# Optimization experiments

Measured on AMD Instinct MI355X. Metric: run time of the kernel, lower is better.

## Reference

```python
import jax, jax.numpy as jnp
import numpy as np

# dims
P, NB, K, NNODES, NPTS, D = 128, 16, 64, 512, 20000, 256
FINEMATCH_MAX_POINT = 450


def setup_inputs() -> dict:
    key = jax.random.key(0)
    k1, k2, k3, k4, k5, k6 = jax.random.split(key, 6)
    ref_node_neighbor_mask = jax.random.uniform(k1, (P, NB)) < 0.9
    ref_node_neighbor_mask = ref_node_neighbor_mask.at[:, 0].set(True)  # ensure no empty proposals
    ref_seed_neighbor_indices = jax.random.randint(k2, (P, NB), 0, NNODES)
    ref_node_knn_masks = jax.random.uniform(k3, (NNODES, K)) < 0.7
    ref_node_knn_masks = ref_node_knn_masks.at[:, 0].set(True)
    ref_node_knn_indices = jax.random.randint(k4, (NNODES, K), 0, NPTS)
    ref_node_knn_points = jax.random.normal(k5, (NNODES, K, 3), dtype=jnp.float32)
    ref_feats_m = jax.random.normal(k6, (NPTS, D), dtype=jnp.float32)
    return {
        'ref_node_neighbor_mask': ref_node_neighbor_mask,
        'ref_seed_neighbor_indices': ref_seed_neighbor_indices,
        'ref_node_knn_masks': ref_node_knn_masks,
        'ref_node_knn_points': ref_node_knn_points,
        'ref_node_knn_indices': ref_node_knn_indices,
        'ref_feats_m': ref_feats_m,
    }


def reference(ref_node_neighbor_mask, ref_seed_neighbor_indices, ref_node_knn_masks,
              ref_node_knn_points, ref_node_knn_indices, ref_feats_m):
    num_proposal, num_neighbors = ref_seed_neighbor_indices.shape
    k = ref_node_knn_masks.shape[-1]
    L = num_neighbors * k
    d = ref_feats_m.shape[-1]
    M = FINEMATCH_MAX_POINT

    # gather per-proposal flattened groups  [P, L]
    corr_masks = ref_node_knn_masks[ref_seed_neighbor_indices].reshape(num_proposal, L)
    corr_points = ref_node_knn_points[ref_seed_neighbor_indices].reshape(num_proposal, L, 3)
    corr_indices = ref_node_knn_indices[ref_seed_neighbor_indices].reshape(num_proposal, L)

    # sentinel feature row (index == NPTS maps to zeros)
    padded_feats = jnp.concatenate([ref_feats_m, jnp.zeros((1, d), ref_feats_m.dtype)], axis=0)
    corr_feats = padded_feats[corr_indices]  # [P, L, D]

    # neighbor mask expand(P, NB, K).reshape(P, NB*K) == repeat each neighbor K times
    nb_mask = jnp.repeat(ref_node_neighbor_mask, k, axis=1)
    corr_masks = jnp.logical_and(corr_masks, nb_mask)

    # per-proposal valid counts and ordered valid positions (stable sort keeps order)
    n = corr_masks.sum(axis=1)  # [P]
    order = jnp.argsort(jnp.logical_not(corr_masks), axis=1)  # valid positions first, in order

    i = jnp.arange(M)
    # resample: floor((i/M) * n) replicates torch float32 linspace resampling
    frac = i.astype(jnp.float32) / jnp.float32(M)
    resampled = jnp.floor(frac[None, :] * n[:, None].astype(jnp.float32)).astype(jnp.int32)
    direct = jnp.broadcast_to(i[None, :].astype(jnp.int32), (num_proposal, M))
    local = jnp.where((n > M)[:, None], resampled, direct)
    out_mask = i[None, :] < jnp.minimum(n, M)[:, None]  # [P, M]
    local = jnp.clip(local, 0, L - 1)

    pos = jnp.take_along_axis(order, local, axis=1)  # [P, M] positions into flattened group
    pts = jnp.take_along_axis(corr_points, pos[:, :, None], axis=1)  # [P, M, 3]
    fts = jnp.take_along_axis(corr_feats, pos[:, :, None], axis=1)   # [P, M, D]
    zero = jnp.zeros((), pts.dtype)
    local_ref_corr_points = jnp.where(out_mask[:, :, None], pts, zero)
    local_ref_corr_feats = jnp.where(out_mask[:, :, None], fts, zero)
    return local_ref_corr_points, local_ref_corr_feats, out_mask
```

## Files before the change

### kernel.cpp

```cpp
#include <hip/hip_runtime.h>

#define NP 128
#define NB 16
#define KK 64
#define LL 1024
#define MM 450
#define DD 256

__device__ __forceinline__ bool probe_is_u8(const void* nb_mask_raw) {
    const unsigned int* w = (const unsigned int*)nb_mask_raw;
    bool u8 = false;
#pragma unroll
    for (int q = 0; q < 16; ++q) u8 |= (w[q] > 1u);
    return u8;
}

__device__ __forceinline__ int read_bool(const void* buf, int idx, bool is_u8) {
    if (is_u8) return ((const unsigned char*)buf)[idx] != 0;
    return ((const int*)buf)[idx] != 0;
}

__global__ __launch_bounds__(256) void n2p_compact(
    const void* __restrict__ nb_mask_raw,
    const int*  __restrict__ seed_idx,
    const void* __restrict__ knn_mask_raw,
    int* __restrict__ ws_order,
    int* __restrict__ ws_n)
{
    const int p = blockIdx.x;
    const int t = threadIdx.x;
    const bool is_u8 = probe_is_u8(nb_mask_raw);

    __shared__ int s_node[NB];
    __shared__ int s_m[NB];
    __shared__ int s_scan[256];

    if (t < NB) {
        s_node[t] = seed_idx[p * NB + t];
        s_m[t]    = read_bool(nb_mask_raw, p * NB + t, is_u8);
    }
    __syncthreads();

    const int base = t * 4;
    int v[4];
    int cnt = 0;
#pragma unroll
    for (int q = 0; q < 4; ++q) {
        const int l  = base + q;
        const int nb = l >> 6;
        const int k  = l & 63;
        const int valid = s_m[nb] && read_bool(knn_mask_raw, s_node[nb] * KK + k, is_u8);
        v[q] = valid;
        cnt += valid;
    }

    s_scan[t] = cnt;
    __syncthreads();
    int val = cnt;
    for (int off = 1; off < 256; off <<= 1) {
        int other = (t >= off) ? s_scan[t - off] : 0;
        __syncthreads();
        val += other;
        s_scan[t] = val;
        __syncthreads();
    }

    if (t == 255) ws_n[p] = val;

    int r = val - cnt;
#pragma unroll
    for (int q = 0; q < 4; ++q) {
        if (v[q]) ws_order[p * LL + (r++)] = base + q;
    }
}

__global__ __launch_bounds__(256) void n2p_gather(
    const int*   __restrict__ seed_idx,
    const float* __restrict__ knn_pts,
    const int*   __restrict__ knn_idx,
    const float* __restrict__ feats,
    const int*   __restrict__ ws_order,
    const int*   __restrict__ ws_n,
    float* __restrict__ out_pts,
    float* __restrict__ out_feats,
    float* __restrict__ out_mask)
{
    const int p    = blockIdx.x;
    const int wave = threadIdx.x >> 6;
    const int lane = threadIdx.x & 63;
    const int i    = blockIdx.y * 4 + wave;
    if (i >= MM) return;

    const int n     = ws_n[p];
    const int n_eff = (n < MM) ? n : MM;
    const size_t row = (size_t)p * MM + i;

    if (i < n_eff) {
        int j;
        if (n > MM) {
            j = (i * n) / MM;
        } else {
            j = i;
        }
        const int l    = ws_order[p * LL + j];
        const int nb   = l >> 6;
        const int k    = l & 63;
        const int node = seed_idx[p * NB + nb];
        const int gk   = node * KK + k;
        const int idx  = knn_idx[gk];

        const float4 f = reinterpret_cast<const float4*>(feats + (size_t)idx * DD)[lane];
        reinterpret_cast<float4*>(out_feats + row * DD)[lane] = f;

        if (lane < 3)  out_pts[row * 3 + lane] = knn_pts[(size_t)gk * 3 + lane];
        if (lane == 0) out_mask[row] = 1.0f;
    } else {
        const float4 z = make_float4(0.f, 0.f, 0.f, 0.f);
        reinterpret_cast<float4*>(out_feats + row * DD)[lane] = z;
        if (lane < 3)  out_pts[row * 3 + lane] = 0.0f;
        if (lane == 0) out_mask[row] = 0.0f;
    }
}

extern "C" void kernel_launch(void* const* d_in, const int* in_sizes, int n_in,
                              void* d_out, int out_size, void* d_ws, size_t ws_size,
                              hipStream_t stream) {
    const void*  nb_mask  = d_in[0];
    const int*   seed_idx = (const int*)d_in[1];
    const void*  knn_mask = d_in[2];
    const float* knn_pts  = (const float*)d_in[3];
    const int*   knn_idx  = (const int*)d_in[4];
    const float* feats    = (const float*)d_in[5];

    float* out_pts   = (float*)d_out;
    float* out_feats = out_pts + (size_t)NP * MM * 3;
    float* out_mask  = out_feats + (size_t)NP * MM * DD;

    int* ws_n     = (int*)d_ws;
    int* ws_order = ws_n + NP;

    n2p_compact<<<dim3(NP), dim3(256), 0, stream>>>(
        nb_mask, seed_idx, knn_mask, ws_order, ws_n);

    n2p_gather<<<dim3(NP, (MM + 3) / 4), dim3(256), 0, stream>>>(
        seed_idx, knn_pts, knn_idx, feats, ws_order, ws_n,
        out_pts, out_feats, out_mask);
}
```

Baseline: 110.7 us.

## Fuse compaction and gather into one kernel with ballot-based scan

```diff
diff --git a/kernel.cpp b/kernel.cpp
--- a/kernel.cpp
+++ b/kernel.cpp
@@ -6,6 +6,8 @@
 #define LL 1024
 #define MM 450
 #define DD 256
+#define CHUNKS 8
+#define ROWS 57
 
 __device__ __forceinline__ bool probe_is_u8(const void* nb_mask_raw) {
     const unsigned int* w = (const unsigned int*)nb_mask_raw;
@@ -20,105 +22,104 @@
     return ((const int*)buf)[idx] != 0;
 }
 
-__global__ __launch_bounds__(256) void n2p_compact(
-    const void* __restrict__ nb_mask_raw,
-    const int*  __restrict__ seed_idx,
-    const void* __restrict__ knn_mask_raw,
-    int* __restrict__ ws_order,
-    int* __restrict__ ws_n)
-{
-    const int p = blockIdx.x;
-    const int t = threadIdx.x;
-    const bool is_u8 = probe_is_u8(nb_mask_raw);
-
-    __shared__ int s_node[NB];
-    __shared__ int s_m[NB];
-    __shared__ int s_scan[256];
-
-    if (t < NB) {
-        s_node[t] = seed_idx[p * NB + t];
-        s_m[t]    = read_bool(nb_mask_raw, p * NB + t, is_u8);
-    }
-    __syncthreads();
-
-    const int base = t * 4;
-    int v[4];
-    int cnt = 0;
-#pragma unroll
-    for (int q = 0; q < 4; ++q) {
-        const int l  = base + q;
-        const int nb = l >> 6;
-        const int k  = l & 63;
-        const int valid = s_m[nb] && read_bool(knn_mask_raw, s_node[nb] * KK + k, is_u8);
-        v[q] = valid;
-        cnt += valid;
-    }
-
-    s_scan[t] = cnt;
-    __syncthreads();
-    int val = cnt;
-    for (int off = 1; off < 256; off <<= 1) {
-        int other = (t >= off) ? s_scan[t - off] : 0;
-        __syncthreads();
-        val += other;
-        s_scan[t] = val;
-        __syncthreads();
-    }
-
-    if (t == 255) ws_n[p] = val;
-
-    int r = val - cnt;
-#pragma unroll
-    for (int q = 0; q < 4; ++q) {
-        if (v[q]) ws_order[p * LL + (r++)] = base + q;
-    }
-}
-
-__global__ __launch_bounds__(256) void n2p_gather(
+__global__ __launch_bounds__(256) void n2p_fused(
+    const void*  __restrict__ nb_mask_raw,
     const int*   __restrict__ seed_idx,
+    const void*  __restrict__ knn_mask_raw,
     const float* __restrict__ knn_pts,
     const int*   __restrict__ knn_idx,
     const float* __restrict__ feats,
-    const int*   __restrict__ ws_order,
-    const int*   __restrict__ ws_n,
     float* __restrict__ out_pts,
     float* __restrict__ out_feats,
     float* __restrict__ out_mask)
 {
-    const int p    = blockIdx.x;
-    const int wave = threadIdx.x >> 6;
-    const int lane = threadIdx.x & 63;
-    const int i    = blockIdx.y * 4 + wave;
-    if (i >= MM) return;
+    const int p     = blockIdx.x;
+    const int chunk = blockIdx.y;
+    const int t     = threadIdx.x;
+    const int wv    = t >> 6;
+    const int ln    = t & 63;
 
-    const int n     = ws_n[p];
-    const int n_eff = (n < MM) ? n : MM;
-    const size_t row = (size_t)p * MM + i;
+    __shared__ int s_node[NB];
+    __shared__ int s_order[LL];
+    __shared__ int s_wsum[4];
+    __shared__ int s_src[ROWS];
+    __shared__ int s_fidx[ROWS];
 
-    if (i < n_eff) {
-        int j;
-        if (n > MM) {
-            j = (i * n) / MM;
+    const bool is_u8 = probe_is_u8(nb_mask_raw);
+
+    if (t < NB) s_node[t] = seed_idx[p * NB + t];
+    __syncthreads();
+
+    int v[4];
+#pragma unroll
+    for (int q = 0; q < 4; ++q) {
+        const int nbi  = wv * 4 + q;
+        const int node = s_node[nbi];
+        const int m_nb = read_bool(nb_mask_raw, p * NB + nbi, is_u8);
+        const int m_kn = read_bool(knn_mask_raw, node * KK + ln, is_u8);
+        v[q] = m_nb && m_kn;
+    }
+    const unsigned long long lt = (1ULL << ln) - 1ULL;
+    int my_rank[4];
+    int wtot = 0;
+#pragma unroll
+    for (int q = 0; q < 4; ++q) {
+        const unsigned long long b = __ballot(v[q] != 0);
+        my_rank[q] = wtot + __popcll(b & lt);
+        wtot += __popcll(b);
+    }
+    if (ln == 0) s_wsum[wv] = wtot;
+    __syncthreads();
+
+    int wave_off = 0;
+    for (int w2 = 0; w2 < wv; ++w2) wave_off += s_wsum[w2];
+    const int n_total = s_wsum[0] + s_wsum[1] + s_wsum[2] + s_wsum[3];
+#pragma unroll
+    for (int q = 0; q < 4; ++q) {
+        if (v[q]) s_order[wave_off + my_rank[q]] = wv * 256 + q * 64 + ln;
+    }
+    __syncthreads();
+
+    const int row0  = chunk * ROWS;
+    const int nrows = (MM - row0 < ROWS) ? (MM - row0) : ROWS;
+    const int n_eff = (n_total < MM) ? n_total : MM;
+
+    if (t < nrows) {
+        const int i = row0 + t;
+        int src = -1, fidx = -1;
+        if (i < n_eff) {
+            const int j = (n_total > MM) ? (int)((unsigned)(i * n_total) / (unsigned)MM)
+                                         : i;
+            const int l    = s_order[j];
+            const int node = s_node[l >> 6];
+            src  = node * KK + (l & 63);
+            fidx = knn_idx[src];
+        }
+        s_src[t]  = src;
+        s_fidx[t] = fidx;
+
+        const size_t row = (size_t)p * MM + i;
+        if (src >= 0) {
+            out_pts[row * 3 + 0] = knn_pts[(size_t)src * 3 + 0];
+            out_pts[row * 3 + 1] = knn_pts[(size_t)src * 3 + 1];
+            out_pts[row * 3 + 2] = knn_pts[(size_t)src * 3 + 2];
+            out_mask[row] = 1.0f;
         } else {
-            j = i;
+            out_pts[row * 3 + 0] = 0.0f;
+            out_pts[row * 3 + 1] = 0.0f;
+            out_pts[row * 3 + 2] = 0.0f;
+            out_mask[row] = 0.0f;
         }
-        const int l    = ws_order[p * LL + j];
-        const int nb   = l >> 6;
-        const int k    = l & 63;
-        const int node = seed_idx[p * NB + nb];
-        const int gk   = node * KK + k;
-        const int idx  = knn_idx[gk];
+    }
+    __syncthreads();
 
-        const float4 f = reinterpret_cast<const float4*>(feats + (size_t)idx * DD)[lane];
-        reinterpret_cast<float4*>(out_feats + row * DD)[lane] = f;
-
-        if (lane < 3)  out_pts[row * 3 + lane] = knn_pts[(size_t)gk * 3 + lane];
-        if (lane == 0) out_mask[row] = 1.0f;
-    } else {
-        const float4 z = make_float4(0.f, 0.f, 0.f, 0.f);
-        reinterpret_cast<float4*>(out_feats + row * DD)[lane] = z;
-        if (lane < 3)  out_pts[row * 3 + lane] = 0.0f;
-        if (lane == 0) out_mask[row] = 0.0f;
+    for (int r = wv; r < nrows; r += 4) {
+        const size_t row = (size_t)p * MM + (row0 + r);
+        const int fidx = s_fidx[r];
+        float4 f = make_float4(0.f, 0.f, 0.f, 0.f);
+        if (fidx >= 0)
+            f = reinterpret_cast<const float4*>(feats + (size_t)fidx * DD)[ln];
+        reinterpret_cast<float4*>(out_feats + row * DD)[ln] = f;
     }
 }
 
@@ -136,13 +137,7 @@
     float* out_feats = out_pts + (size_t)NP * MM * 3;
     float* out_mask  = out_feats + (size_t)NP * MM * DD;
 
-    int* ws_n     = (int*)d_ws;
-    int* ws_order = ws_n + NP;
-
-    n2p_compact<<<dim3(NP), dim3(256), 0, stream>>>(
-        nb_mask, seed_idx, knn_mask, ws_order, ws_n);
-
-    n2p_gather<<<dim3(NP, (MM + 3) / 4), dim3(256), 0, stream>>>(
-        seed_idx, knn_pts, knn_idx, feats, ws_order, ws_n,
+    n2p_fused<<<dim3(NP, CHUNKS), dim3(256), 0, stream>>>(
+        nb_mask, seed_idx, knn_mask, knn_pts, knn_idx, feats,
         out_pts, out_feats, out_mask);
 }
```

Measured after the change: 104.6 us. 1.06x faster.
